# Kernel optimization log

Measured on AMD Instinct MI355X. Metric: run time of the kernel, lower is better.

Reference implementation:

```python
import jax, jax.numpy as jnp
import numpy as np

V, E, H, M, C = 50000, 300, 256, 512, 20  # vocab, emb_dim, hid_dim, max_dim, n_classes
S, B = 512, 64  # seq_len, batch


def setup_inputs() -> dict:
    key = jax.random.key(0)
    ks = jax.random.split(key, 16)
    s = lambda i, shape: jax.random.normal(ks[i], shape, dtype=jnp.float32) * 0.05
    return dict(
        inp=jax.random.randint(ks[0], (S, B), 0, V),
        emb_table=s(1, (V, E)),
        c_l0=s(2, (H,)), c_r0=s(3, (H,)),
        W_l_w=s(4, (H, H)), W_l_b=s(5, (H,)),
        W_r_w=s(6, (H, H)), W_r_b=s(7, (H,)),
        W_sl_w=s(8, (H, E)), W_sl_b=s(9, (H,)),
        W_sr_w=s(10, (H, E)), W_sr_b=s(11, (H,)),
        max_w=s(12, (M, 2 * H + E)), max_b=s(13, (M,)),
        doc_w=s(14, (C, M)), doc_b=s(15, (C,)),
    )


def reference(inp, emb_table, c_l0, c_r0, W_l_w, W_l_b, W_r_w, W_r_b,
              W_sl_w, W_sl_b, W_sr_w, W_sr_b, max_w, max_b, doc_w, doc_b):
    emb = emb_table[inp]  # [S, B, E]
    # precomputed per-token projections (batched once, as in the original)
    emb_ls = jnp.einsum('sbe,he->sbh', emb, W_sl_w) + W_sl_b  # [S, B, H]
    emb_rs = jnp.einsum('sbe,he->sbh', emb, W_sr_w) + W_sr_b  # [S, B, H]

    batch = inp.shape[1]

    def make_step(W, b):
        def step(c, x):  # c: [B, H], x: [B, H]
            c = jnp.tanh(c @ W.T + b + x)
            return c, c
        return step

    c0_l = jnp.broadcast_to(c_l0, (batch, c_l0.shape[0]))
    c0_r = jnp.broadcast_to(c_r0, (batch, c_r0.shape[0]))
    _, c_ls = jax.lax.scan(make_step(W_l_w, W_l_b), c0_l, emb_ls)          # left-to-right
    _, c_rs = jax.lax.scan(make_step(W_r_w, W_r_b), c0_r, emb_rs[::-1])    # right-to-left
    c_rs = c_rs[::-1]  # re-align to original time order (stack(c_rs[::-1]))

    cat = jnp.concatenate([c_ls, emb, c_rs], axis=-1)  # [S, B, 2H+E]
    y = jnp.tanh(jnp.einsum('sbc,mc->sbm', cat, max_w) + max_b)  # [S, B, M]
    y_max = jnp.max(y, axis=0)  # [B, M] element-wise max-pool over time
    return jax.nn.log_softmax(y_max @ doc_w.T + doc_b, axis=-1)  # [B, C]
```

## Files before the change

### kernel.cpp

```cpp
#include <hip/hip_runtime.h>
#include <hip/hip_bf16.h>

constexpr int kS = 512;
constexpr int kB = 64;
constexpr int kE = 300;
constexpr int kH = 256;
constexpr int kM = 512;
constexpr int kC = 20;

typedef short s16x8 __attribute__((ext_vector_type(8)));
typedef float f32x4 __attribute__((ext_vector_type(4)));
typedef unsigned short u16x4 __attribute__((ext_vector_type(4)));
typedef _Float16 f16x8 __attribute__((ext_vector_type(8)));
typedef __fp16 hf16x2 __attribute__((ext_vector_type(2)));

__device__ __forceinline__ float fast_tanh(float z) {
    z = fminf(15.f, fmaxf(-15.f, z));
    float e = __expf(2.f * z);
    return 1.f - 2.f / (e + 1.f);
}

__device__ __forceinline__ unsigned short f2bf(float f) {
    __hip_bfloat16 h = __float2bfloat16(f);
    return *(unsigned short*)&h;
}
union F16U { _Float16 h; unsigned short u; };
__device__ __forceinline__ unsigned short f16bits(_Float16 h) { F16U x; x.h = h; return x.u; }

__device__ __forceinline__ void lds_barrier() {
    asm volatile("s_waitcnt lgkmcnt(0)\n\ts_barrier" ::: "memory");
}


__global__ __launch_bounds__(256) void prepw_kernel(
    const float* __restrict__ max_w,
    const float* __restrict__ wsl, const float* __restrict__ wsr,
    const float* __restrict__ wl, const float* __restrict__ wr,
    unsigned short* __restrict__ Wmax, unsigned short* __restrict__ Wproj,
    unsigned short* __restrict__ Wscan)
{
    int idx = blockIdx.x * 256 + threadIdx.x;
    if (idx < 512 * 832) {
        int r = idx / 832, c = idx - r * 832;
        float v;
        if (c < 556)      v = max_w[r * 812 + c];
        else if (c < 576) v = 0.f;
        else              v = max_w[r * 812 + (c - 20)];
        Wmax[idx] = f2bf(v);
    }
    if (idx < 512 * 320) {
        int r = idx / 320, c = idx - r * 320;
        float v = 0.f;
        if (c < 300) v = (r < 256) ? wsl[r * 300 + c] : wsr[(r - 256) * 300 + c];
        Wproj[idx] = f2bf(v);
    }
    if (idx < 2 * 256 * 256) {
        int d = idx >> 16, rc = idx & 65535;
        float v = (d ? wr : wl)[rc];
        Wscan[idx] = f16bits((_Float16)v);
    }
}

__global__ __launch_bounds__(128) void gather_kernel(
    const int* __restrict__ inp, const float* __restrict__ emb_table,
    unsigned short* __restrict__ E)
{
    const int row = blockIdx.x;
    const int b = row >> 9, s = row & 511;
    const int t = threadIdx.x;
    unsigned short* dst = E + (size_t)row * 320;
    const int v = inp[s * kB + b];
    const float* src = emb_table + (size_t)v * kE;
    if (t < 75) {
        float4 f = *(const float4*)&src[t * 4];
        u16x4 o = { f2bf(f.x), f2bf(f.y), f2bf(f.z), f2bf(f.w) };
        *(u16x4*)&dst[t * 4] = o;
    } else if (t < 80) {
        u16x4 z = { 0, 0, 0, 0 };
        *(u16x4*)&dst[300 + (t - 75) * 4] = z;
    }
}

__global__ __launch_bounds__(256) void proj_mfma_kernel(
    const unsigned short* __restrict__ E,
    const unsigned short* __restrict__ Wproj,
    const float* __restrict__ b_sl, const float* __restrict__ b_sr,
    unsigned short* __restrict__ XCL, unsigned short* __restrict__ XCR)
{
    __shared__ unsigned short As[128 * 40];
    __shared__ unsigned short Bs[128 * 40];
    const int tid = threadIdx.x;
    const int row0 = blockIdx.x * 128;
    const int col0 = blockIdx.y * 128;
    const int lane = tid & 63;
    const int wave = tid >> 6;
    const int wr = (wave >> 1) * 64, wc = (wave & 1) * 64;
    const int l15 = lane & 15, lk = (lane >> 4) * 8;
    const int srow = tid >> 1;
    const int sh = (tid & 1) * 16;

    const unsigned short* Ag = E + (size_t)(row0 + srow) * 320 + sh;
    const unsigned short* Bg = Wproj + (size_t)(col0 + srow) * 320 + sh;

    f32x4 acc[4][4] = {};
    float4 av0 = *(const float4*)Ag;
    float4 av1 = *(const float4*)(Ag + 8);
    float4 bv0 = *(const float4*)Bg;
    float4 bv1 = *(const float4*)(Bg + 8);

    for (int kk = 0; kk < 10; ++kk) {
        __syncthreads();
        *(float4*)&As[srow * 40 + sh] = av0;
        *(float4*)&As[srow * 40 + sh + 8] = av1;
        *(float4*)&Bs[srow * 40 + sh] = bv0;
        *(float4*)&Bs[srow * 40 + sh + 8] = bv1;
        __syncthreads();
        if (kk < 9) {
            av0 = *(const float4*)(Ag + (kk + 1) * 32);
            av1 = *(const float4*)(Ag + (kk + 1) * 32 + 8);
            bv0 = *(const float4*)(Bg + (kk + 1) * 32);
            bv1 = *(const float4*)(Bg + (kk + 1) * 32 + 8);
        }
        s16x8 af[4], bf[4];
#pragma unroll
        for (int f = 0; f < 4; ++f) {
            af[f] = *(const s16x8*)&As[(wr + f * 16 + l15) * 40 + lk];
            bf[f] = *(const s16x8*)&Bs[(wc + f * 16 + l15) * 40 + lk];
        }
#pragma unroll
        for (int i = 0; i < 4; ++i)
#pragma unroll
            for (int j = 0; j < 4; ++j)
                acc[i][j] = __builtin_amdgcn_mfma_f32_16x16x32_bf16(af[i], bf[j], acc[i][j], 0, 0, 0);
    }

    const int rbase = row0 + wr + (lane >> 4) * 4;
#pragma unroll
    for (int j = 0; j < 4; ++j) {
        const int col = col0 + wc + j * 16 + l15;
        const float bias = (col < kH) ? b_sl[col] : b_sr[col - kH];
        unsigned short* X = (col < kH) ? XCL : XCR;
        const int ccol = col & 255;
#pragma unroll
        for (int i = 0; i < 4; ++i) {
#pragma unroll
            for (int r = 0; r < 4; ++r) {
                const int row = rbase + i * 16 + r;
                const int s = row & 511, b = row >> 9;
                X[((size_t)s * 64 + b) * 256 + ccol] = f2bf(acc[i][j][r] + bias);
            }
        }
    }
}

__global__ __launch_bounds__(512, 2) void scan_mfma_kernel(
    const float* __restrict__ c_l0, const float* __restrict__ c_r0,
    const float* __restrict__ b_l, const float* __restrict__ b_r,
    const unsigned short* __restrict__ Wscan,
    unsigned short* __restrict__ XCL, unsigned short* __restrict__ XCR)
{
    __shared__ unsigned short cF[2][16 * 256];

    const int dir = blockIdx.x >> 2;
    const int bg  = blockIdx.x & 3;
    const int tid = threadIdx.x;
    const int lane = tid & 63;
    const int wave = tid >> 6;
    const int l15 = lane & 15;
    const int q4  = lane >> 4;
    const int n0  = wave * 32;

    const float* bias = dir ? b_r : b_l;
    const float* c0v  = dir ? c_r0 : c_l0;
    const unsigned short* W = Wscan + (dir << 16);
    unsigned short* XC = dir ? XCR : XCL;

    f16x8 wf[2][8];
#pragma unroll
    for (int j = 0; j < 2; ++j)
#pragma unroll
        for (int ks = 0; ks < 8; ++ks)
            wf[j][ks] = *(const f16x8*)&W[(n0 + j * 16 + l15) * 256 + ks * 32 + q4 * 8];

    float biasv[2][4];
#pragma unroll
    for (int j = 0; j < 2; ++j)
#pragma unroll
        for (int r = 0; r < 4; ++r)
            biasv[j][r] = bias[n0 + j * 16 + q4 * 4 + r];

    const unsigned int base0 = (unsigned)((bg * 16 + l15) * 256 + n0 + q4 * 4);

    int ridx[8], widx[2];
#pragma unroll
    for (int ks = 0; ks < 8; ++ks)
        ridx[ks] = (l15 * 256 + ks * 32 + q4 * 8) ^ ((l15 & 7) << 3);
#pragma unroll
    for (int j = 0; j < 2; ++j)
        widx[j] = (l15 * 256 + n0 + j * 16 + q4 * 4) ^ ((l15 & 7) << 3);

    if (tid < 256) {
        unsigned short hb = f16bits((_Float16)c0v[tid]);
        for (int row = 0; row < 16; ++row)
            cF[0][(row * 256 + tid) ^ ((row & 7) << 3)] = hb;
    }

    const int s0i = dir ? 511 : 0;
    const int s1i = dir ? 510 : 1;
    uint2 xa[2], xb[2];
#pragma unroll
    for (int j = 0; j < 2; ++j) {
        xa[j] = *(const uint2*)(XC + base0 + (unsigned)s0i * 16384u + j * 16);
        xb[j] = *(const uint2*)(XC + base0 + (unsigned)s1i * 16384u + j * 16);
    }
    lds_barrier();

    auto body = [&](int t, uint2 (&xc)[2]) {
        const int st = dir ? (511 - t) : t;
        const int sld = dir ? (st - 2 < 0 ? 0 : st - 2)
                            : (st + 2 > 511 ? 511 : st + 2);
        const int p = t & 1;

        f32x4 acc[2], acc2[2];
#pragma unroll
        for (int j = 0; j < 2; ++j) {
            const unsigned d0 = xc[j].x, d1 = xc[j].y;
            acc[j][0] = biasv[j][0]; acc[j][1] = biasv[j][1];
            acc[j][2] = biasv[j][2]; acc[j][3] = biasv[j][3];
            acc2[j][0] = __uint_as_float(d0 << 16);
            acc2[j][1] = __uint_as_float(d0 & 0xffff0000u);
            acc2[j][2] = __uint_as_float(d1 << 16);
            acc2[j][3] = __uint_as_float(d1 & 0xffff0000u);
        }

#pragma unroll
        for (int j = 0; j < 2; ++j)
            xc[j] = *(const uint2*)(XC + base0 + (unsigned)sld * 16384u + j * 16);

        f16x8 ah[8];
#pragma unroll
        for (int ks = 0; ks < 8; ++ks)
            ah[ks] = *(const f16x8*)&cF[p][ridx[ks]];
#pragma unroll
        for (int ks = 0; ks < 4; ++ks) {
            acc[0]  = __builtin_amdgcn_mfma_f32_16x16x32_f16(wf[0][ks],     ah[ks],     acc[0],  0, 0, 0);
            acc[1]  = __builtin_amdgcn_mfma_f32_16x16x32_f16(wf[1][ks],     ah[ks],     acc[1],  0, 0, 0);
            acc2[0] = __builtin_amdgcn_mfma_f32_16x16x32_f16(wf[0][ks + 4], ah[ks + 4], acc2[0], 0, 0, 0);
            acc2[1] = __builtin_amdgcn_mfma_f32_16x16x32_f16(wf[1][ks + 4], ah[ks + 4], acc2[1], 0, 0, 0);
        }

#pragma unroll
        for (int j = 0; j < 2; ++j) {
            float t0, t1, t2, t3;
            {
                float z0 = acc[j][0] + acc2[j][0];
                float z1 = acc[j][1] + acc2[j][1];
                float z2 = acc[j][2] + acc2[j][2];
                float z3 = acc[j][3] + acc2[j][3];
                float e0 = __builtin_amdgcn_exp2f(z0 * 2.8853900817779268f);
                float e1 = __builtin_amdgcn_exp2f(z1 * 2.8853900817779268f);
                float e2 = __builtin_amdgcn_exp2f(z2 * 2.8853900817779268f);
                float e3 = __builtin_amdgcn_exp2f(z3 * 2.8853900817779268f);
                t0 = fmaf(-2.f, __builtin_amdgcn_rcpf(e0 + 1.f), 1.f);
                t1 = fmaf(-2.f, __builtin_amdgcn_rcpf(e1 + 1.f), 1.f);
                t2 = fmaf(-2.f, __builtin_amdgcn_rcpf(e2 + 1.f), 1.f);
                t3 = fmaf(-2.f, __builtin_amdgcn_rcpf(e3 + 1.f), 1.f);
            }
            union { hf16x2 h; unsigned u; } h0, h1;
            h0.h = __builtin_amdgcn_cvt_pkrtz(t0, t1);
            h1.h = __builtin_amdgcn_cvt_pkrtz(t2, t3);
            uint2 hw; hw.x = h0.u; hw.y = h1.u;
            *(uint2*)&cF[p ^ 1][widx[j]] = hw;
            uint2 pkb;
            asm("v_cvt_pk_bf16_f32 %0, %1, %2" : "=v"(pkb.x) : "v"(t0), "v"(t1));
            asm("v_cvt_pk_bf16_f32 %0, %1, %2" : "=v"(pkb.y) : "v"(t2), "v"(t3));
            *(uint2*)(XC + base0 + (unsigned)st * 16384u + j * 16) = pkb;
        }
        lds_barrier();
    };

    for (int t = 0; t < kS; t += 2) {
        body(t, xa);
        body(t + 1, xb);
    }
}

__global__ __launch_bounds__(256) void maxlayer_mfma_kernel(
    const unsigned short* __restrict__ XCL, const unsigned short* __restrict__ E,
    const unsigned short* __restrict__ XCR, const unsigned short* __restrict__ Wmax,
    float* __restrict__ part_max)
{
    __shared__ unsigned short As[128 * 40];
    __shared__ unsigned short Bs[128 * 40];
    __shared__ float red[2][128];
    const int tid = threadIdx.x;
    const int mt = blockIdx.x, sc = blockIdx.y, b = blockIdx.z;
    const int col0 = mt * 128;
    const int lane = tid & 63;
    const int wave = tid >> 6;
    const int wrow = wave >> 1;
    const int wr = wrow * 64, wc = (wave & 1) * 64;
    const int l15 = lane & 15, lk = (lane >> 4) * 8;
    const int srow = tid >> 1;
    const int sh = (tid & 1) * 16;

    const int s = sc * 128 + srow;
    const unsigned short* baseL = XCL + ((size_t)s * 64 + b) * 256 + sh;
    const unsigned short* baseE = E + (size_t)(b * 512 + s) * 320 + sh;
    const unsigned short* baseR = XCR + ((size_t)s * 64 + b) * 256 + sh;
    const unsigned short* Bg = Wmax + (size_t)(col0 + srow) * 832 + sh;

    auto aptr = [&](int kk) -> const unsigned short* {
        if (kk < 8)  return baseL + kk * 32;
        if (kk < 18) return baseE + (kk - 8) * 32;
        return baseR + (kk - 18) * 32;
    };

    f32x4 acc[4][4] = {};
    float4 av0 = *(const float4*)aptr(0);
    float4 av1 = *(const float4*)(aptr(0) + 8);
    float4 bv0 = *(const float4*)Bg;
    float4 bv1 = *(const float4*)(Bg + 8);

    for (int kk = 0; kk < 26; ++kk) {
        __syncthreads();
        *(float4*)&As[srow * 40 + sh] = av0;
        *(float4*)&As[srow * 40 + sh + 8] = av1;
        *(float4*)&Bs[srow * 40 + sh] = bv0;
        *(float4*)&Bs[srow * 40 + sh + 8] = bv1;
        __syncthreads();
        if (kk < 25) {
            const unsigned short* ap = aptr(kk + 1);
            av0 = *(const float4*)ap;
            av1 = *(const float4*)(ap + 8);
            bv0 = *(const float4*)(Bg + (kk + 1) * 32);
            bv1 = *(const float4*)(Bg + (kk + 1) * 32 + 8);
        }
        s16x8 af[4], bf[4];
#pragma unroll
        for (int f = 0; f < 4; ++f) {
            af[f] = *(const s16x8*)&As[(wr + f * 16 + l15) * 40 + lk];
            bf[f] = *(const s16x8*)&Bs[(wc + f * 16 + l15) * 40 + lk];
        }
#pragma unroll
        for (int i = 0; i < 4; ++i)
#pragma unroll
            for (int j = 0; j < 4; ++j)
                acc[i][j] = __builtin_amdgcn_mfma_f32_16x16x32_bf16(af[i], bf[j], acc[i][j], 0, 0, 0);
    }

#pragma unroll
    for (int j = 0; j < 4; ++j) {
        float m = -1e30f;
#pragma unroll
        for (int i = 0; i < 4; ++i)
#pragma unroll
            for (int r = 0; r < 4; ++r) m = fmaxf(m, acc[i][j][r]);
        m = fmaxf(m, __shfl_xor(m, 16));
        m = fmaxf(m, __shfl_xor(m, 32));
        if (lane < 16) red[wrow][wc + j * 16 + lane] = m;
    }
    __syncthreads();
    if (tid < 128) {
        float v = fmaxf(red[0][tid], red[1][tid]);
        part_max[((size_t)(b * 4 + sc)) * kM + col0 + tid] = v;
    }
}

__global__ __launch_bounds__(256) void final_kernel(
    const float* __restrict__ part_max, const float* __restrict__ max_b,
    const float* __restrict__ doc_w, const float* __restrict__ doc_b,
    float* __restrict__ out)
{
    const int b = blockIdx.x;
    const int t = threadIdx.x;
    __shared__ float ym[kM];
    __shared__ float red[160];
    __shared__ float logits[kC];

    for (int m = t; m < kM; m += 256) {
        float v = -1e30f;
        for (int ch = 0; ch < 4; ++ch)
            v = fmaxf(v, part_max[((size_t)(b * 4 + ch)) * kM + m]);
        ym[m] = fast_tanh(v + max_b[m]);
    }
    __syncthreads();
    if (t < 160) {
        int c = t >> 3, kg = t & 7;
        float s = 0.f;
        const float* wr = doc_w + c * kM + kg * 64;
        const float* yr = ym + kg * 64;
        for (int k = 0; k < 64; ++k) s += yr[k] * wr[k];
        red[t] = s;
    }
    __syncthreads();
    if (t < kC) {
        float s = doc_b[t];
        for (int kg = 0; kg < 8; ++kg) s += red[t * 8 + kg];
        logits[t] = s;
    }
    __syncthreads();
    if (t == 0) {
        float mx = logits[0];
        for (int c = 1; c < kC; ++c) mx = fmaxf(mx, logits[c]);
        float se = 0.f;
        for (int c = 0; c < kC; ++c) se += __expf(logits[c] - mx);
        float lse = mx + __logf(se);
        for (int c = 0; c < kC; ++c) out[b * kC + c] = logits[c] - lse;
    }
}

extern "C" void kernel_launch(void* const* d_in, const int* in_sizes, int n_in,
                              void* d_out, int out_size, void* d_ws, size_t ws_size,
                              hipStream_t stream) {
    const int* inp = (const int*)d_in[0];
    const float* emb_table = (const float*)d_in[1];
    const float* c_l0 = (const float*)d_in[2];
    const float* c_r0 = (const float*)d_in[3];
    const float* W_l_w = (const float*)d_in[4];
    const float* W_l_b = (const float*)d_in[5];
    const float* W_r_w = (const float*)d_in[6];
    const float* W_r_b = (const float*)d_in[7];
    const float* W_sl_w = (const float*)d_in[8];
    const float* W_sl_b = (const float*)d_in[9];
    const float* W_sr_w = (const float*)d_in[10];
    const float* W_sr_b = (const float*)d_in[11];
    const float* max_w = (const float*)d_in[12];
    const float* max_b = (const float*)d_in[13];
    const float* doc_w = (const float*)d_in[14];
    const float* doc_b = (const float*)d_in[15];
    float* out = (float*)d_out;

    char* w = (char*)d_ws;
    unsigned short* E     = (unsigned short*)(w);
    unsigned short* XCL   = (unsigned short*)(w + 20971520);
    unsigned short* XCR   = (unsigned short*)(w + 37748736);
    unsigned short* Wmax  = (unsigned short*)(w + 54525952);
    unsigned short* Wproj = (unsigned short*)(w + 55377920);
    float* part_max       = (float*)(w + 55705600);
    unsigned short* Wscan = (unsigned short*)(w + 56229888);

    prepw_kernel<<<(512 * 832 + 255) / 256, 256, 0, stream>>>(
        max_w, W_sl_w, W_sr_w, W_l_w, W_r_w, Wmax, Wproj, Wscan);
    gather_kernel<<<kS * kB, 128, 0, stream>>>(inp, emb_table, E);
    proj_mfma_kernel<<<dim3(256, 4), 256, 0, stream>>>(
        E, Wproj, W_sl_b, W_sr_b, XCL, XCR);
    scan_mfma_kernel<<<8, 512, 0, stream>>>(
        c_l0, c_r0, W_l_b, W_r_b, Wscan, XCL, XCR);
    maxlayer_mfma_kernel<<<dim3(4, 4, 64), 256, 0, stream>>>(
        XCL, E, XCR, Wmax, part_max);
    final_kernel<<<kB, 256, 0, stream>>>(part_max, max_b, doc_w, doc_b, out);
}
```

Measured before the change: 519.5 us.

## Fold recurrent bias into projection and halve scan block to four waves

The recurrent biases b_l/b_r are added once per token in the projection epilogue, so the scan no longer keeps per-lane bias registers or adds them each step. The scan kernel drops from 8 waves to 4 waves per block. Each wave now owns 64 hidden columns and holds twice as many weight fragments in registers. This cuts cross-wave synchronisation and LDS traffic per timestep on the serial critical path, at the cost of more MFMA work and register pressure per wave. Bias is now rounded to bf16 together with the projection, which slightly changes precision.

```diff
diff --git a/kernel.cpp b/kernel.cpp
--- a/kernel.cpp
+++ b/kernel.cpp
@@ -85,6 +85,7 @@
     const unsigned short* __restrict__ E,
     const unsigned short* __restrict__ Wproj,
     const float* __restrict__ b_sl, const float* __restrict__ b_sr,
+    const float* __restrict__ b_l, const float* __restrict__ b_r,
     unsigned short* __restrict__ XCL, unsigned short* __restrict__ XCR)
 {
     __shared__ unsigned short As[128 * 40];
@@ -138,7 +139,8 @@
 #pragma unroll
     for (int j = 0; j < 4; ++j) {
         const int col = col0 + wc + j * 16 + l15;
-        const float bias = (col < kH) ? b_sl[col] : b_sr[col - kH];
+        const float bias = (col < kH) ? (b_sl[col] + b_l[col])
+                                      : (b_sr[col - kH] + b_r[col - kH]);
         unsigned short* X = (col < kH) ? XCL : XCR;
         const int ccol = col & 255;
 #pragma unroll
@@ -153,9 +155,8 @@
     }
 }
 
-__global__ __launch_bounds__(512, 2) void scan_mfma_kernel(
+__global__ __launch_bounds__(256) void scan_mfma_kernel(
     const float* __restrict__ c_l0, const float* __restrict__ c_r0,
-    const float* __restrict__ b_l, const float* __restrict__ b_r,
     const unsigned short* __restrict__ Wscan,
     unsigned short* __restrict__ XCL, unsigned short* __restrict__ XCR)
 {
@@ -168,38 +169,30 @@
     const int wave = tid >> 6;
     const int l15 = lane & 15;
     const int q4  = lane >> 4;
-    const int n0  = wave * 32;
-
-    const float* bias = dir ? b_r : b_l;
+    const int n0  = wave * 64;
+
     const float* c0v  = dir ? c_r0 : c_l0;
     const unsigned short* W = Wscan + (dir << 16);
     unsigned short* XC = dir ? XCR : XCL;
 
-    f16x8 wf[2][8];
-#pragma unroll
-    for (int j = 0; j < 2; ++j)
+    f16x8 wf[4][8];
+#pragma unroll
+    for (int j = 0; j < 4; ++j)
 #pragma unroll
         for (int ks = 0; ks < 8; ++ks)
             wf[j][ks] = *(const f16x8*)&W[(n0 + j * 16 + l15) * 256 + ks * 32 + q4 * 8];
 
-    float biasv[2][4];
-#pragma unroll
-    for (int j = 0; j < 2; ++j)
-#pragma unroll
-        for (int r = 0; r < 4; ++r)
-            biasv[j][r] = bias[n0 + j * 16 + q4 * 4 + r];
-
     const unsigned int base0 = (unsigned)((bg * 16 + l15) * 256 + n0 + q4 * 4);
 
-    int ridx[8], widx[2];
+    int ridx[8], widx[4];
 #pragma unroll
     for (int ks = 0; ks < 8; ++ks)
         ridx[ks] = (l15 * 256 + ks * 32 + q4 * 8) ^ ((l15 & 7) << 3);
 #pragma unroll
-    for (int j = 0; j < 2; ++j)
+    for (int j = 0; j < 4; ++j)
         widx[j] = (l15 * 256 + n0 + j * 16 + q4 * 4) ^ ((l15 & 7) << 3);
 
-    if (tid < 256) {
+    {
         unsigned short hb = f16bits((_Float16)c0v[tid]);
         for (int row = 0; row < 16; ++row)
             cF[0][(row * 256 + tid) ^ ((row & 7) << 3)] = hb;
@@ -207,34 +200,33 @@
 
     const int s0i = dir ? 511 : 0;
     const int s1i = dir ? 510 : 1;
-    uint2 xa[2], xb[2];
-#pragma unroll
-    for (int j = 0; j < 2; ++j) {
+    uint2 xa[4], xb[4];
+#pragma unroll
+    for (int j = 0; j < 4; ++j) {
         xa[j] = *(const uint2*)(XC + base0 + (unsigned)s0i * 16384u + j * 16);
         xb[j] = *(const uint2*)(XC + base0 + (unsigned)s1i * 16384u + j * 16);
     }
     lds_barrier();
 
-    auto body = [&](int t, uint2 (&xc)[2]) {
+    auto body = [&](int t, uint2 (&xc)[4]) {
         const int st = dir ? (511 - t) : t;
         const int sld = dir ? (st - 2 < 0 ? 0 : st - 2)
                             : (st + 2 > 511 ? 511 : st + 2);
         const int p = t & 1;
 
-        f32x4 acc[2], acc2[2];
-#pragma unroll
-        for (int j = 0; j < 2; ++j) {
+        f32x4 acc[4], acc2[4];
+#pragma unroll
+        for (int j = 0; j < 4; ++j) {
             const unsigned d0 = xc[j].x, d1 = xc[j].y;
-            acc[j][0] = biasv[j][0]; acc[j][1] = biasv[j][1];
-            acc[j][2] = biasv[j][2]; acc[j][3] = biasv[j][3];
-            acc2[j][0] = __uint_as_float(d0 << 16);
-            acc2[j][1] = __uint_as_float(d0 & 0xffff0000u);
-            acc2[j][2] = __uint_as_float(d1 << 16);
-            acc2[j][3] = __uint_as_float(d1 & 0xffff0000u);
-        }
-
-#pragma unroll
-        for (int j = 0; j < 2; ++j)
+            acc[j][0] = __uint_as_float(d0 << 16);
+            acc[j][1] = __uint_as_float(d0 & 0xffff0000u);
+            acc[j][2] = __uint_as_float(d1 << 16);
+            acc[j][3] = __uint_as_float(d1 & 0xffff0000u);
+            acc2[j][0] = 0.f; acc2[j][1] = 0.f; acc2[j][2] = 0.f; acc2[j][3] = 0.f;
+        }
+
+#pragma unroll
+        for (int j = 0; j < 4; ++j)
             xc[j] = *(const uint2*)(XC + base0 + (unsigned)sld * 16384u + j * 16);
 
         f16x8 ah[8];
@@ -243,14 +235,15 @@
             ah[ks] = *(const f16x8*)&cF[p][ridx[ks]];
 #pragma unroll
         for (int ks = 0; ks < 4; ++ks) {
-            acc[0]  = __builtin_amdgcn_mfma_f32_16x16x32_f16(wf[0][ks],     ah[ks],     acc[0],  0, 0, 0);
-            acc[1]  = __builtin_amdgcn_mfma_f32_16x16x32_f16(wf[1][ks],     ah[ks],     acc[1],  0, 0, 0);
-            acc2[0] = __builtin_amdgcn_mfma_f32_16x16x32_f16(wf[0][ks + 4], ah[ks + 4], acc2[0], 0, 0, 0);
-            acc2[1] = __builtin_amdgcn_mfma_f32_16x16x32_f16(wf[1][ks + 4], ah[ks + 4], acc2[1], 0, 0, 0);
-        }
-
-#pragma unroll
-        for (int j = 0; j < 2; ++j) {
+#pragma unroll
+            for (int j = 0; j < 4; ++j) {
+                acc[j]  = __builtin_amdgcn_mfma_f32_16x16x32_f16(wf[j][ks],     ah[ks],     acc[j],  0, 0, 0);
+                acc2[j] = __builtin_amdgcn_mfma_f32_16x16x32_f16(wf[j][ks + 4], ah[ks + 4], acc2[j], 0, 0, 0);
+            }
+        }
+
+#pragma unroll
+        for (int j = 0; j < 4; ++j) {
             float t0, t1, t2, t3;
             {
                 float z0 = acc[j][0] + acc2[j][0];
@@ -444,9 +437,9 @@
         max_w, W_sl_w, W_sr_w, W_l_w, W_r_w, Wmax, Wproj, Wscan);
     gather_kernel<<<kS * kB, 128, 0, stream>>>(inp, emb_table, E);
     proj_mfma_kernel<<<dim3(256, 4), 256, 0, stream>>>(
-        E, Wproj, W_sl_b, W_sr_b, XCL, XCR);
-    scan_mfma_kernel<<<8, 512, 0, stream>>>(
-        c_l0, c_r0, W_l_b, W_r_b, Wscan, XCL, XCR);
+        E, Wproj, W_sl_b, W_sr_b, W_l_b, W_r_b, XCL, XCR);
+    scan_mfma_kernel<<<8, 256, 0, stream>>>(
+        c_l0, c_r0, Wscan, XCL, XCR);
     maxlayer_mfma_kernel<<<dim3(4, 4, 64), 256, 0, stream>>>(
         XCL, E, XCR, Wmax, part_max);
     final_kernel<<<kB, 256, 0, stream>>>(part_max, max_b, doc_w, doc_b, out);
```

New measurement: 595.2 us. 14.6% more time.
